# Performance work log

Measured on AMD Instinct MI355X. Metric: run time of the kernel, lower is better.

The kernel has to match this reference:

```python
import jax, jax.numpy as jnp
import numpy as np

HEADS = 8
HEAD_DIM = 64
IN_DIM = HEADS * HEAD_DIM  # 512
SCALE = HEAD_DIM ** (-0.5)


def _split_heads(t):
    # [b, n, h*d] -> [b, h, n, d]
    b, n, _ = t.shape
    return t.reshape(b, n, HEADS, HEAD_DIM).transpose(0, 2, 1, 3)


def _merge_heads(t):
    # [b, h, n, d] -> [b, n, h*d]
    b, h, n, d = t.shape
    return t.transpose(0, 2, 1, 3).reshape(b, n, h * d)


def setup_inputs() -> dict:
    key = jax.random.key(0)
    ks = jax.random.split(key, 6)
    b, n = 8, 1024
    nv = jax.random.normal(ks[0], (b, n, IN_DIM), dtype=jnp.float32)
    rv = jax.random.normal(ks[1], (b, n, IN_DIM), dtype=jnp.float32)
    s = IN_DIM ** (-0.5)
    W_noise = jax.random.normal(ks[2], (IN_DIM, 2 * IN_DIM), dtype=jnp.float32) * s
    b_noise = jnp.zeros((2 * IN_DIM,), dtype=jnp.float32)
    W_rgb = jax.random.normal(ks[3], (IN_DIM, 2 * IN_DIM), dtype=jnp.float32) * s
    b_rgb = jnp.zeros((2 * IN_DIM,), dtype=jnp.float32)
    return {"nv": nv, "rv": rv, "W_noise": W_noise, "b_noise": b_noise,
            "W_rgb": W_rgb, "b_rgb": b_rgb}


def reference(nv, rv, W_noise, b_noise, W_rgb, b_rgb):
    # qk projections, chunk(2, dim=-1)
    nqk = nv @ W_noise + b_noise                      # [b, n, 2*in_dim]
    noise_q, noise_k = jnp.split(nqk, 2, axis=-1)
    rqk = rv @ W_rgb + b_rgb
    rgb_q, rgb_k = jnp.split(rqk, 2, axis=-1)

    noise_q, noise_k = _split_heads(noise_q), _split_heads(noise_k)  # [b,h,n,d]
    rgb_q, rgb_k = _split_heads(rgb_q), _split_heads(rgb_k)

    attn1 = jnp.einsum('bhnd,bhmd->bhnm', noise_q, rgb_k) * SCALE
    attn2 = jnp.einsum('bhnd,bhmd->bhnm', rgb_q, noise_k) * SCALE

    # NOTE: original uses nn.Softmax(dim=1) => softmax over the HEADS axis.
    attn1 = jax.nn.softmax(attn1, axis=1)
    attn2 = jax.nn.softmax(attn2, axis=1)

    rv_h = _split_heads(rv)  # values are the raw inputs, not projections
    nv_h = _split_heads(nv)

    noise = jnp.einsum('bhnm,bhmd->bhnd', attn1, rv_h)
    rgb = jnp.einsum('bhnm,bhmd->bhnd', attn2, nv_h)

    return (_merge_heads(noise), _merge_heads(rgb))
```

## Files before the change

### kernel.cpp

```cpp
#include <hip/hip_runtime.h>
#include <hip/hip_bf16.h>

typedef __attribute__((ext_vector_type(8))) short short8;
typedef __attribute__((ext_vector_type(4))) short short4v;
typedef __attribute__((ext_vector_type(4))) float float4v;

#define MFMA16(a, b, c) __builtin_amdgcn_mfma_f32_16x16x32_bf16(a, b, c, 0, 0, 0)

__device__ __forceinline__ short f2bf(float f) {
    __hip_bfloat16 hb = __float2bfloat16(f);
    return *reinterpret_cast<short*>(&hb);
}
__device__ __forceinline__ float bf2f(short s) {
    __hip_bfloat16 hb = *reinterpret_cast<__hip_bfloat16*>(&s);
    return __bfloat162float(hb);
}

__global__ __launch_bounds__(256) void prep_kernel(
    const float* __restrict__ nv, const float* __restrict__ rv,
    const float* __restrict__ Wn, const float* __restrict__ Wr,
    __hip_bfloat16* __restrict__ Vtn, __hip_bfloat16* __restrict__ Vtr,
    __hip_bfloat16* __restrict__ An,  __hip_bfloat16* __restrict__ Ar,
    __hip_bfloat16* __restrict__ Wtn, __hip_bfloat16* __restrict__ Wtr)
{
    __shared__ short lds[64][72];
    const int t = threadIdx.x;

    if (blockIdx.z == 8) {
        const int id = blockIdx.x + 32 * blockIdx.y;
        const int c0 = (id & 15) * 64;
        const int k0 = ((id >> 4) & 7) * 64;
        const int g  = id >> 7;
        const float* W = g ? Wr : Wn;
        __hip_bfloat16* Wt = g ? Wtr : Wtn;
        {
            const int i  = t >> 2;
            const int j0 = (t & 3) * 16;
            const float* p = W + (size_t)(k0 + i) * 1024 + c0 + j0;
            #pragma unroll
            for (int jj = 0; jj < 16; ++jj)
                lds[j0 + jj][i] = f2bf(p[jj]);
        }
        __syncthreads();
        {
            const int j  = t >> 2;
            const int i0 = (t & 3) * 16;
            __hip_bfloat16* q = Wt + (size_t)(c0 + j) * 512 + k0 + i0;
            short8 v0 = *reinterpret_cast<const short8*>(&lds[j][i0]);
            short8 v1 = *reinterpret_cast<const short8*>(&lds[j][i0 + 8]);
            *reinterpret_cast<short8*>(q)     = v0;
            *reinterpret_cast<short8*>(q + 8) = v1;
        }
        return;
    }

    const int ntile = blockIdx.x & 15;
    const int src   = blockIdx.x >> 4;
    const int h     = blockIdx.y;
    const int b     = blockIdx.z;
    const float* V  = src ? rv : nv;
    __hip_bfloat16* Vt = src ? Vtr : Vtn;
    __hip_bfloat16* Ab = src ? Ar  : An;

    const int n0 = ntile * 64;
    {
        const int i  = t >> 2;
        const int j0 = (t & 3) * 16;
        const float* p = V + ((size_t)(b * 1024) + n0 + i) * 512 + h * 64 + j0;
        short8 a0, a1;
        #pragma unroll
        for (int jj = 0; jj < 8; ++jj) {
            short x = f2bf(p[jj]);
            a0[jj] = x; lds[j0 + jj][i] = x;
        }
        #pragma unroll
        for (int jj = 0; jj < 8; ++jj) {
            short x = f2bf(p[8 + jj]);
            a1[jj] = x; lds[j0 + 8 + jj][i] = x;
        }
        __hip_bfloat16* adst = Ab + ((size_t)(b * 1024) + n0 + i) * 512 + h * 64 + j0;
        *reinterpret_cast<short8*>(adst)     = a0;
        *reinterpret_cast<short8*>(adst + 8) = a1;
    }
    __syncthreads();
    {
        const int j  = t >> 2;
        const int i0 = (t & 3) * 16;
        __hip_bfloat16* q = Vt + (((size_t)(b * 8 + h) * 64) + j) * 1024 + n0 + i0;
        short8 v0 = *reinterpret_cast<const short8*>(&lds[j][i0]);
        short8 v1 = *reinterpret_cast<const short8*>(&lds[j][i0 + 8]);
        *reinterpret_cast<short8*>(q)     = v0;
        *reinterpret_cast<short8*>(q + 8) = v1;
    }
}

__global__ __launch_bounds__(256, 4) void proj_kernel(
    const __hip_bfloat16* __restrict__ An, const __hip_bfloat16* __restrict__ Ar,
    const __hip_bfloat16* __restrict__ Wtn, const __hip_bfloat16* __restrict__ Wtr,
    const float* __restrict__ bn, const float* __restrict__ br,
    __hip_bfloat16* __restrict__ Qn, __hip_bfloat16* __restrict__ Kn,
    __hip_bfloat16* __restrict__ Qr, __hip_bfloat16* __restrict__ Kr)
{
    const int m0 = blockIdx.x * 64;
    const int c0 = blockIdx.y * 256;
    const int g  = blockIdx.z;
    const __hip_bfloat16* A  = g ? Ar  : An;
    const __hip_bfloat16* Wt = g ? Wtr : Wtn;
    const float* bias = g ? br : bn;
    __hip_bfloat16* Qd = g ? Qr : Qn;
    __hip_bfloat16* Kd = g ? Kr : Kn;

    __shared__ short Bt[2][4][256][8];

    const int t    = threadIdx.x;
    const int lane = t & 63;
    const int w    = t >> 6;
    const int l15  = lane & 15;
    const int lg   = lane >> 4;

    auto stage = [&](int buf, int kk) {
        #pragma unroll
        for (int rep = 0; rep < 4; ++rep) {
            const int u = rep * 256 + t;
            const int s = u >> 8;
            const int c = u & 255;
            const __hip_bfloat16* src = Wt + (size_t)(c0 + c) * 512 + kk + s * 8;
            __builtin_amdgcn_global_load_lds(
                (const __attribute__((address_space(1))) unsigned int*)src,
                (__attribute__((address_space(3))) unsigned int*)&Bt[buf][s][c][0],
                16, 0, 0);
        }
    };

    float4v acc[16] = {};
    const int mrow = m0 + w * 16 + l15;

    stage(0, 0);
    __syncthreads();

    for (int kk = 0; kk < 512; kk += 32) {
        const int buf = (kk >> 5) & 1;
        if (kk < 480) stage(buf ^ 1, kk + 32);
        short8 afrag = *reinterpret_cast<const short8*>(
            A + (size_t)mrow * 512 + kk + lg * 8);
        #pragma unroll
        for (int cs = 0; cs < 16; ++cs) {
            short8 bfrag = *reinterpret_cast<const short8*>(
                &Bt[buf][lg][cs * 16 + l15][0]);
            acc[cs] = MFMA16(afrag, bfrag, acc[cs]);
        }
        __syncthreads();
    }

    #pragma unroll
    for (int cs = 0; cs < 16; ++cs) {
        const int c  = c0 + cs * 16 + l15;
        const bool isK = (c >= 512);
        const int hh = (c >> 6) & 7;
        const int d  = c & 63;
        __hip_bfloat16* dst = isK ? Kd : Qd;
        const float bv = bias[c];
        #pragma unroll
        for (int r = 0; r < 4; ++r) {
            const int m = m0 + w * 16 + lg * 4 + r;
            const int b = m >> 10, n = m & 1023;
            dst[(((size_t)(b * 8 + hh) * 1024 + n) * 64) + d] =
                __float2bfloat16(acc[cs][r] + bv);
        }
    }
}

__global__ __launch_bounds__(512, 2) void attn_kernel(
    const __hip_bfloat16* __restrict__ Qn, const __hip_bfloat16* __restrict__ Kn,
    const __hip_bfloat16* __restrict__ Qr, const __hip_bfloat16* __restrict__ Kr,
    const __hip_bfloat16* __restrict__ Vtn, const __hip_bfloat16* __restrict__ Vtr,
    float* __restrict__ out)
{
    const int combo = blockIdx.x;
    const int bb    = combo & 7;
    const int dir   = combo >> 3;
    const int nt    = blockIdx.y;
    const __hip_bfloat16* Q  = dir ? Qr  : Qn;
    const __hip_bfloat16* K  = dir ? Kn  : Kr;
    const __hip_bfloat16* Vt = dir ? Vtn : Vtr;
    float* O = out + (size_t)dir * (8u * 1024u * 512u);

    const int t    = threadIdx.x;
    const int lane = t & 63;
    const int w    = t >> 6;
    const int iw   = w & 1;
    const int hg   = w >> 1;
    const int h0   = hg * 2;
    const int l15  = lane & 15;
    const int lg   = lane >> 4;

    __shared__ short K_s[8 * 32 * 64];
    __shared__ short P_s[8][32][40];
    __shared__ short Xb[2][4][2][64][8];

    const int n0 = nt * 64;
    const float C = 0.125f * 1.44269504f;

    const __hip_bfloat16* Vb[2] = {
        Vt + (size_t)((bb * 8 + h0)     * 64) * 1024,
        Vt + (size_t)((bb * 8 + h0 + 1) * 64) * 1024 };

    auto stage = [&](int mt) {
        #pragma unroll
        for (int i = 0; i < 4; ++i) {
            const int u    = (w * 4 + i) * 64 + lane;
            const int h    = u >> 8;
            const int mr   = (u >> 3) & 31;
            const int slot = (u & 7) ^ (mr & 7);
            const __hip_bfloat16* g =
                K + ((size_t)((bb * 8 + h) * 1024) + mt + mr) * 64 + slot * 8;
            __builtin_amdgcn_global_load_lds(
                (const __attribute__((address_space(1))) unsigned int*)g,
                (__attribute__((address_space(3))) unsigned int*)&K_s[u * 8],
                16, 0, 0);
        }
    };

    short8 qf[2][2][2];
    #pragma unroll
    for (int ns = 0; ns < 2; ++ns)
        #pragma unroll
        for (int hh = 0; hh < 2; ++hh)
            #pragma unroll
            for (int kc = 0; kc < 2; ++kc)
                qf[ns][hh][kc] = *reinterpret_cast<const short8*>(
                    Q + ((size_t)((bb * 8 + h0 + hh) * 1024) + n0 + ns * 32 + iw * 16 + l15) * 64
                      + kc * 32 + lg * 8);

    float4v oacc[2][2][4] = {};

    stage(0);
    __syncthreads();

    for (int it = 0; it < 32; ++it) {
        const int m0 = it << 5;
        short8 vf[2][4];
        #pragma unroll
        for (int hh = 0; hh < 2; ++hh)
            #pragma unroll
            for (int dd = 0; dd < 4; ++dd)
                vf[hh][dd] = *reinterpret_cast<const short8*>(
                    Vb[hh] + (size_t)(dd * 16 + l15) * 1024 + m0 + lg * 8);
        short8 kf[2][2][2];
        #pragma unroll
        for (int hh = 0; hh < 2; ++hh)
            #pragma unroll
            for (int j = 0; j < 2; ++j) {
                const int mr = j * 16 + l15;
                #pragma unroll
                for (int kc = 0; kc < 2; ++kc)
                    kf[hh][j][kc] = *reinterpret_cast<const short8*>(
                        K_s + (h0 + hh) * 2048 + mr * 64
                            + (((kc * 4 + lg) ^ (mr & 7)) * 8));
            }

        #pragma unroll
        for (int ns = 0; ns < 2; ++ns) {
            float4v sacc[2][2] = {};
            #pragma unroll
            for (int hh = 0; hh < 2; ++hh)
                #pragma unroll
                for (int j = 0; j < 2; ++j)
                    #pragma unroll
                    for (int kc = 0; kc < 2; ++kc)
                        sacc[hh][j] = MFMA16(kf[hh][j][kc], qf[ns][hh][kc], sacc[hh][j]);
            float e[2][8];
            float ps[8] = {0.f, 0.f, 0.f, 0.f, 0.f, 0.f, 0.f, 0.f};
            #pragma unroll
            for (int hh = 0; hh < 2; ++hh)
                #pragma unroll
                for (int j = 0; j < 2; ++j)
                    #pragma unroll
                    for (int r = 0; r < 4; ++r) {
                        float ev = exp2f(sacc[hh][j][r] * C);
                        e[hh][j * 4 + r] = ev;
                        ps[j * 4 + r] += ev;
                    }
            {
                short8 pk;
                #pragma unroll
                for (int p = 0; p < 8; ++p) pk[p] = f2bf(ps[p]);
                *reinterpret_cast<short8*>(&Xb[ns][hg][iw][lane][0]) = pk;
            }
            __syncthreads();
            if (ns == 0)
                stage((it < 31) ? m0 + 32 : 0);
            float inv[8];
            {
                float tot[8];
                #pragma unroll
                for (int p = 0; p < 8; ++p) tot[p] = ps[p];
                #pragma unroll
                for (int g = 1; g < 4; ++g) {
                    short8 x = *reinterpret_cast<const short8*>(
                        &Xb[ns][(hg + g) & 3][iw][lane][0]);
                    #pragma unroll
                    for (int p = 0; p < 8; ++p) tot[p] += bf2f(x[p]);
                }
                #pragma unroll
                for (int p = 0; p < 8; ++p)
                    inv[p] = __builtin_amdgcn_rcpf(tot[p]);
            }
            #pragma unroll
            for (int hh = 0; hh < 2; ++hh)
                #pragma unroll
                for (int j = 0; j < 2; ++j) {
                    short4v pk;
                    #pragma unroll
                    for (int r = 0; r < 4; ++r)
                        pk[r] = f2bf(e[hh][j * 4 + r] * inv[j * 4 + r]);
                    *reinterpret_cast<short4v*>(
                        &P_s[h0 + hh][iw * 16 + l15][j * 16 + lg * 4]) = pk;
                }
            #pragma unroll
            for (int hh = 0; hh < 2; ++hh) {
                short8 pf = *reinterpret_cast<const short8*>(
                    &P_s[h0 + hh][iw * 16 + l15][lg * 8]);
                #pragma unroll
                for (int dd = 0; dd < 4; ++dd)
                    oacc[ns][hh][dd] = MFMA16(pf, vf[hh][dd], oacc[ns][hh][dd]);
            }
        }
        __syncthreads();
    }

    #pragma unroll
    for (int ns = 0; ns < 2; ++ns)
        #pragma unroll
        for (int hh = 0; hh < 2; ++hh)
            #pragma unroll
            for (int dd = 0; dd < 4; ++dd)
                #pragma unroll
                for (int r = 0; r < 4; ++r) {
                    const int n = n0 + ns * 32 + iw * 16 + lg * 4 + r;
                    const int d = dd * 16 + l15;
                    O[((size_t)(bb * 1024) + n) * 512 + (h0 + hh) * 64 + d] =
                        oacc[ns][hh][dd][r];
                }
}

extern "C" void kernel_launch(void* const* d_in, const int* in_sizes, int n_in,
                              void* d_out, int out_size, void* d_ws, size_t ws_size,
                              hipStream_t stream) {
    const float* nv = (const float*)d_in[0];
    const float* rv = (const float*)d_in[1];
    const float* Wn = (const float*)d_in[2];
    const float* bn = (const float*)d_in[3];
    const float* Wr = (const float*)d_in[4];
    const float* br = (const float*)d_in[5];
    float* out = (float*)d_out;

    __hip_bfloat16* w = (__hip_bfloat16*)d_ws;
    const size_t E = 8ull * 8 * 1024 * 64;
    __hip_bfloat16* Qn  = w;
    __hip_bfloat16* Kn  = w + E;
    __hip_bfloat16* Qr  = w + 2 * E;
    __hip_bfloat16* Kr  = w + 3 * E;
    __hip_bfloat16* Vtn = w + 4 * E;
    __hip_bfloat16* Vtr = w + 5 * E;
    __hip_bfloat16* An  = w + 6 * E;
    __hip_bfloat16* Ar  = w + 7 * E;
    __hip_bfloat16* Wtn = w + 8 * E;
    __hip_bfloat16* Wtr = w + 8 * E + 512 * 1024;

    prep_kernel<<<dim3(32, 8, 9), 256, 0, stream>>>(nv, rv, Wn, Wr,
                                                    Vtn, Vtr, An, Ar, Wtn, Wtr);
    proj_kernel<<<dim3(128, 4, 2), 256, 0, stream>>>(An, Ar, Wtn, Wtr, bn, br,
                                                     Qn, Kn, Qr, Kr);
    attn_kernel<<<dim3(16, 16), 512, 0, stream>>>(Qn, Kn, Qr, Kr, Vtn, Vtr, out);
}
```

Before: 175.8 us.

## Split attention key range across two warp groups with LDS reduction

Doubles the attention block to 1024 threads and splits the 1024-key loop into two halves, each handled by a separate group of 8 waves with its own K, P and partial-sum LDS buffers. The two partial output accumulators are combined through shared memory before one group writes the result. The grid stays at 256 blocks, so this raises per-CU wave count and latency hiding without adding blocks. The cost is a larger LDS footprint, block-wide barriers that now span 16 waves, and an extra reduction step at the end.

```diff
diff --git a/kernel.cpp b/kernel.cpp
--- a/kernel.cpp
+++ b/kernel.cpp
@@ -170,7 +170,7 @@
     }
 }
 
-__global__ __launch_bounds__(512, 2) void attn_kernel(
+__global__ __launch_bounds__(1024, 1) void attn_kernel(
     const __hip_bfloat16* __restrict__ Qn, const __hip_bfloat16* __restrict__ Kn,
     const __hip_bfloat16* __restrict__ Qr, const __hip_bfloat16* __restrict__ Kr,
     const __hip_bfloat16* __restrict__ Vtn, const __hip_bfloat16* __restrict__ Vtr,
@@ -188,17 +188,20 @@
     const int t    = threadIdx.x;
     const int lane = t & 63;
     const int w    = t >> 6;
-    const int iw   = w & 1;
-    const int hg   = w >> 1;
+    const int mh   = w >> 3;
+    const int wl   = w & 7;
+    const int iw   = wl & 1;
+    const int hg   = wl >> 1;
     const int h0   = hg * 2;
     const int l15  = lane & 15;
     const int lg   = lane >> 4;
 
-    __shared__ short K_s[8 * 32 * 64];
-    __shared__ short P_s[8][32][40];
-    __shared__ short Xb[2][4][2][64][8];
+    __shared__ short K_s[2][8 * 32 * 64];
+    __shared__ short P_s[2][8][32][40];
+    __shared__ short Xb[2][2][4][2][64][8];
 
     const int n0 = nt * 64;
+    const int mbase = mh * 512;
     const float C = 0.125f * 1.44269504f;
 
     const __hip_bfloat16* Vb[2] = {
@@ -208,7 +211,7 @@
     auto stage = [&](int mt) {
         #pragma unroll
         for (int i = 0; i < 4; ++i) {
-            const int u    = (w * 4 + i) * 64 + lane;
+            const int u    = (wl * 4 + i) * 64 + lane;
             const int h    = u >> 8;
             const int mr   = (u >> 3) & 31;
             const int slot = (u & 7) ^ (mr & 7);
@@ -216,7 +219,7 @@
                 K + ((size_t)((bb * 8 + h) * 1024) + mt + mr) * 64 + slot * 8;
             __builtin_amdgcn_global_load_lds(
                 (const __attribute__((address_space(1))) unsigned int*)g,
-                (__attribute__((address_space(3))) unsigned int*)&K_s[u * 8],
+                (__attribute__((address_space(3))) unsigned int*)&K_s[mh][u * 8],
                 16, 0, 0);
         }
     };
@@ -234,11 +237,11 @@
 
     float4v oacc[2][2][4] = {};
 
-    stage(0);
+    stage(mbase);
     __syncthreads();
 
-    for (int it = 0; it < 32; ++it) {
-        const int m0 = it << 5;
+    for (int it = 0; it < 16; ++it) {
+        const int m0 = mbase + (it << 5);
         short8 vf[2][4];
         #pragma unroll
         for (int hh = 0; hh < 2; ++hh)
@@ -247,6 +250,7 @@
                 vf[hh][dd] = *reinterpret_cast<const short8*>(
                     Vb[hh] + (size_t)(dd * 16 + l15) * 1024 + m0 + lg * 8);
         short8 kf[2][2][2];
+        const short* ks = K_s[mh];
         #pragma unroll
         for (int hh = 0; hh < 2; ++hh)
             #pragma unroll
@@ -255,8 +259,8 @@
                 #pragma unroll
                 for (int kc = 0; kc < 2; ++kc)
                     kf[hh][j][kc] = *reinterpret_cast<const short8*>(
-                        K_s + (h0 + hh) * 2048 + mr * 64
-                            + (((kc * 4 + lg) ^ (mr & 7)) * 8));
+                        ks + (h0 + hh) * 2048 + mr * 64
+                           + (((kc * 4 + lg) ^ (mr & 7)) * 8));
             }
 
         #pragma unroll
@@ -285,11 +289,11 @@
                 short8 pk;
                 #pragma unroll
                 for (int p = 0; p < 8; ++p) pk[p] = f2bf(ps[p]);
-                *reinterpret_cast<short8*>(&Xb[ns][hg][iw][lane][0]) = pk;
+                *reinterpret_cast<short8*>(&Xb[mh][ns][hg][iw][lane][0]) = pk;
             }
             __syncthreads();
             if (ns == 0)
-                stage((it < 31) ? m0 + 32 : 0);
+                stage((it < 15) ? m0 + 32 : mbase);
             float inv[8];
             {
                 float tot[8];
@@ -298,7 +302,7 @@
                 #pragma unroll
                 for (int g = 1; g < 4; ++g) {
                     short8 x = *reinterpret_cast<const short8*>(
-                        &Xb[ns][(hg + g) & 3][iw][lane][0]);
+                        &Xb[mh][ns][(hg + g) & 3][iw][lane][0]);
                     #pragma unroll
                     for (int p = 0; p < 8; ++p) tot[p] += bf2f(x[p]);
                 }
@@ -315,12 +319,12 @@
                     for (int r = 0; r < 4; ++r)
                         pk[r] = f2bf(e[hh][j * 4 + r] * inv[j * 4 + r]);
                     *reinterpret_cast<short4v*>(
-                        &P_s[h0 + hh][iw * 16 + l15][j * 16 + lg * 4]) = pk;
+                        &P_s[mh][h0 + hh][iw * 16 + l15][j * 16 + lg * 4]) = pk;
                 }
             #pragma unroll
             for (int hh = 0; hh < 2; ++hh) {
                 short8 pf = *reinterpret_cast<const short8*>(
-                    &P_s[h0 + hh][iw * 16 + l15][lg * 8]);
+                    &P_s[mh][h0 + hh][iw * 16 + l15][lg * 8]);
                 #pragma unroll
                 for (int dd = 0; dd < 4; ++dd)
                     oacc[ns][hh][dd] = MFMA16(pf, vf[hh][dd], oacc[ns][hh][dd]);
@@ -329,19 +333,49 @@
         __syncthreads();
     }
 
+    float* sc = reinterpret_cast<float*>(&K_s[0][0]);
+    __syncthreads();
     #pragma unroll
-    for (int ns = 0; ns < 2; ++ns)
-        #pragma unroll
-        for (int hh = 0; hh < 2; ++hh)
-            #pragma unroll
-            for (int dd = 0; dd < 4; ++dd)
-                #pragma unroll
-                for (int r = 0; r < 4; ++r) {
-                    const int n = n0 + ns * 32 + iw * 16 + lg * 4 + r;
-                    const int d = dd * 16 + l15;
-                    O[((size_t)(bb * 1024) + n) * 512 + (h0 + hh) * 64 + d] =
-                        oacc[ns][hh][dd][r];
-                }
+    for (int ns = 0; ns < 2; ++ns) {
+        if (mh == 1) {
+            #pragma unroll
+            for (int hh = 0; hh < 2; ++hh)
+                #pragma unroll
+                for (int dd = 0; dd < 4; ++dd)
+                    #pragma unroll
+                    for (int r = 0; r < 4; ++r)
+                        sc[(wl * 32 + hh * 16 + dd * 4 + r) * 64 + lane] =
+                            oacc[ns][hh][dd][r];
+        }
+        __syncthreads();
+        if (mh == 0) {
+            #pragma unroll
+            for (int hh = 0; hh < 2; ++hh)
+                #pragma unroll
+                for (int dd = 0; dd < 4; ++dd)
+                    #pragma unroll
+                    for (int r = 0; r < 4; ++r)
+                        oacc[ns][hh][dd][r] +=
+                            sc[(wl * 32 + hh * 16 + dd * 4 + r) * 64 + lane];
+        }
+        __syncthreads();
+    }
+
+    if (mh == 0) {
+        #pragma unroll
+        for (int ns = 0; ns < 2; ++ns)
+            #pragma unroll
+            for (int hh = 0; hh < 2; ++hh)
+                #pragma unroll
+                for (int dd = 0; dd < 4; ++dd)
+                    #pragma unroll
+                    for (int r = 0; r < 4; ++r) {
+                        const int n = n0 + ns * 32 + iw * 16 + lg * 4 + r;
+                        const int d = dd * 16 + l15;
+                        O[((size_t)(bb * 1024) + n) * 512 + (h0 + hh) * 64 + d] =
+                            oacc[ns][hh][dd][r];
+                    }
+    }
 }
 
 extern "C" void kernel_launch(void* const* d_in, const int* in_sizes, int n_in,
@@ -372,5 +406,5 @@
                                                     Vtn, Vtr, An, Ar, Wtn, Wtr);
     proj_kernel<<<dim3(128, 4, 2), 256, 0, stream>>>(An, Ar, Wtn, Wtr, bn, br,
                                                      Qn, Kn, Qr, Kr);
-    attn_kernel<<<dim3(16, 16), 512, 0, stream>>>(Qn, Kn, Qr, Kr, Vtn, Vtr, out);
-}
+    attn_kernel<<<dim3(16, 16), 1024, 0, stream>>>(Qn, Kn, Qr, Kr, Vtn, Vtr, out);
+}
```

New measurement: 520.7 us. 2.96x slower.
